# Kernel optimization log

Measured on AMD Instinct MI355X. Metric: run time of the kernel, lower is better.

Reference implementation:

```python
import jax, jax.numpy as jnp
import numpy as np


def setup_inputs() -> dict:
    key = jax.random.key(0)
    k1, k2, k3, k4 = jax.random.split(key, 4)
    B, G, C, T = 4, 40, 13, 1024
    return {
        "x": jax.random.normal(k1, (B, G, C, T), dtype=jnp.float32),
        "query_w": jax.random.normal(k2, (C, C), dtype=jnp.float32),
        "key_w": jax.random.normal(k3, (C, C), dtype=jnp.float32),
        "value_w": jax.random.normal(k4, (C, C), dtype=jnp.float32),
    }


def reference(x, query_w, key_w, value_w):
    # x: [B, 40, 13, T] real -> rfft over time -> [B, 40, 13, F] complex
    x_fft = jnp.fft.rfft(x, axis=-1)
    cdt = x_fft.dtype
    wq = query_w.astype(cdt)  # [13,13] complex (zero imag), shared across the 40 groups
    wk = key_w.astype(cdt)
    wv = value_w.astype(cdt)
    xt = jnp.swapaxes(x_fft, -1, -2)  # [B, 40, F, 13]
    q = xt @ wq                       # [B, 40, F, 13]
    k = xt @ wk
    v = xt @ wv
    scores = jnp.abs(q @ jnp.swapaxes(k, -1, -2))     # [B, 40, F, F] real
    attn = jax.nn.softmax(scores, axis=-1).astype(cdt)
    out = (attn @ v)                                   # [B, 40, F, 13]
    out = jnp.swapaxes(out, -1, -2)                    # [B, 40, 13, F]
    return jnp.fft.irfft(out, axis=-1)                 # [B, 40, 13, 2*(F-1)]
```

## Files before the change

kernel.cpp:

```cpp
#include <hip/hip_runtime.h>
#include <math.h>

#define BDIM 4
#define GDIM 40
#define CDIM 13
#define TDIM 1024
#define FDIM 513
#define BG   (BDIM*GDIM)
#define NROW (BG*FDIM)
#define NCHUNK 9
#define TK 64

typedef _Float16 half4 __attribute__((ext_vector_type(4)));
typedef _Float16 half8 __attribute__((ext_vector_type(8)));
typedef float    f32x4 __attribute__((ext_vector_type(4)));

#define MFMA16(a, b, c) __builtin_amdgcn_mfma_f32_16x16x16f16((a), (b), (c), 0, 0, 0)

__device__ __forceinline__ unsigned bitrev10(unsigned x) { return __brev(x) >> 22; }

__global__ void fft_fwd2(const float* __restrict__ x, float2* __restrict__ xf) {
    __shared__ float re[1024], im[1024];
    const int s2 = blockIdx.x;
    const float* x1 = x + (size_t)(2 * s2) * TDIM;
    const float* x2 = x1 + TDIM;
    for (int t = threadIdx.x; t < 1024; t += blockDim.x) {
        unsigned r = bitrev10(t);
        re[r] = x1[t];
        im[r] = x2[t];
    }
    __syncthreads();
    for (int s = 0; s < 10; ++s) {
        int half = 1 << s;
        for (int j = threadIdx.x; j < 512; j += blockDim.x) {
            int grp = j >> s;
            int pos = j & (half - 1);
            int i1 = (grp << (s + 1)) + pos;
            int i2 = i1 + half;
            float ang = -(float)M_PI * (float)pos / (float)half;
            float sw, cw; __sincosf(ang, &sw, &cw);
            float xr = re[i2], xi = im[i2];
            float tr = cw * xr - sw * xi;
            float ti = cw * xi + sw * xr;
            float ur = re[i1], ui = im[i1];
            re[i1] = ur + tr; im[i1] = ui + ti;
            re[i2] = ur - tr; im[i2] = ui - ti;
        }
        __syncthreads();
    }
    const int sigA = 2 * s2, sigB = sigA + 1;
    const int bgA = sigA / CDIM, cA = sigA % CDIM;
    const int bgB = sigB / CDIM, cB = sigB % CDIM;
    for (int f = threadIdx.x; f < FDIM; f += blockDim.x) {
        int fr = (1024 - f) & 1023;
        float zr = re[f], zi = im[f];
        float wr = re[fr], wi = im[fr];
        xf[((size_t)bgA * FDIM + f) * CDIM + cA] =
            make_float2(0.5f * (zr + wr), 0.5f * (zi - wi));
        xf[((size_t)bgB * FDIM + f) * CDIM + cB] =
            make_float2(0.5f * (zi + wi), 0.5f * (wr - zr));
    }
}

__global__ void qkv_kernel(const float2* __restrict__ xf,
                           const float* __restrict__ wq,
                           const float* __restrict__ wk,
                           const float* __restrict__ wv,
                           float2* __restrict__ q,
                           _Float16* __restrict__ KP,
                           _Float16* __restrict__ VT) {
    int gid = blockIdx.x * blockDim.x + threadIdx.x;
    if (gid >= NROW * CDIM) return;
    int r = gid / CDIM;
    int i = gid - r * CDIM;
    const float2* xrow = xf + (size_t)r * CDIM;
    float qr = 0, qi = 0, kr = 0, ki = 0, vr = 0, vi = 0;
#pragma unroll
    for (int c = 0; c < CDIM; ++c) {
        float2 xc = xrow[c];
        float a = wq[c * CDIM + i]; qr += xc.x * a; qi += xc.y * a;
        float b = wk[c * CDIM + i]; kr += xc.x * b; ki += xc.y * b;
        float d = wv[c * CDIM + i]; vr += xc.x * d; vi += xc.y * d;
    }
    q[gid] = make_float2(qr, qi);

    _Float16* krow = KP + (size_t)r * 64;
    _Float16 h0 = (_Float16)kr;
    _Float16 h1 = (_Float16)ki;
    krow[i]      = h0;
    krow[13 + i] = h1;
    krow[32 + i] = (_Float16)(kr - (float)h0);
    krow[45 + i] = (_Float16)(ki - (float)h1);
    if (i == 12) {
        *(unsigned int*)(krow + 26) = 0u;
        *(unsigned int*)(krow + 28) = 0u;
        *(unsigned int*)(krow + 30) = 0u;
        *(unsigned int*)(krow + 58) = 0u;
        *(unsigned int*)(krow + 60) = 0u;
        *(unsigned int*)(krow + 62) = 0u;
    }
    int bg = r / FDIM;
    int f  = r - bg * FDIM;
    VT[((size_t)(bg * 2 + 0) * 16 + i) * 520 + f] = (_Float16)vr;
    VT[((size_t)(bg * 2 + 1) * 16 + i) * 520 + f] = (_Float16)vi;
}

__global__ __launch_bounds__(256, 4) void attn_kernel(const float2* __restrict__ q,
                                                      const _Float16* __restrict__ KP,
                                                      const _Float16* __restrict__ VT,
                                                      float2* __restrict__ outspec) {
    __shared__ __align__(16) _Float16 Klds[TK * 64];
    __shared__ __align__(16) _Float16 VTlds[2 * 16 * 72];

    const int bg    = blockIdx.x / NCHUNK;
    const int chunk = blockIdx.x % NCHUNK;
    const int tid   = threadIdx.x;
    const int w     = tid >> 6;
    const int lane  = tid & 63;
    const int qlane = lane & 15;
    const int g     = lane >> 4;
    const int frow  = chunk * 64 + w * 16 + qlane;
    const bool writer = (frow < FDIM);
    const int f     = writer ? frow : (FDIM - 1);
    const size_t rowbase = (size_t)(bg * FDIM + f) * CDIM;

    half4 uh[2], ul[2], u2h[2], u2l[2];
#pragma unroll
    for (int c01 = 0; c01 < 2; ++c01) {
#pragma unroll
        for (int j = 0; j < 4; ++j) {
            int k = c01 * 16 + 4 * g + j;
            float a = 0.f, b = 0.f;
            if (k < CDIM) {
                float2 t = q[rowbase + k];          a = t.x;  b = t.y;
            } else if (k < 2 * CDIM) {
                float2 t = q[rowbase + (k - CDIM)]; a = -t.y; b = t.x;
            }
            _Float16 ah = (_Float16)a;
            uh[c01][j]  = ah;
            ul[c01][j]  = (_Float16)(a - (float)ah);
            _Float16 bh = (_Float16)b;
            u2h[c01][j] = bh;
            u2l[c01][j] = (_Float16)(b - (float)bh);
        }
    }

    f32x4 o_re = {0.f, 0.f, 0.f, 0.f};
    f32x4 o_im = {0.f, 0.f, 0.f, 0.f};
    float m = -INFINITY, l = 0.f;

    const _Float16* __restrict__ KPg = KP + (size_t)bg * FDIM * 64;
    const _Float16* __restrict__ VTg = VT + (size_t)bg * 2 * 16 * 520;

    for (int t0 = 0; t0 < FDIM; t0 += TK) {
        __syncthreads();
#pragma unroll
        for (int hh = 0; hh < 2; ++hh) {
            int gr  = tid + hh * 256;
            int krw = gr >> 3, gg = gr & 7;
            half8 val;
#pragma unroll
            for (int e = 0; e < 8; ++e) val[e] = (_Float16)0.f;
            int grow = t0 + krw;
            if (grow < FDIM)
                val = *(const half8*)(KPg + (size_t)grow * 64 + gg * 8);
            *(half8*)(Klds + krw * 64 + ((gg ^ (krw & 7)) << 3)) = val;
        }
        {
            int gk = tid & 7, cc = (tid >> 3) & 15, part = tid >> 7;
            int rb = t0 + gk * 8;
            half8 val;
#pragma unroll
            for (int e = 0; e < 8; ++e) val[e] = (_Float16)0.f;
            if (rb < FDIM) {
                val = *(const half8*)(VTg + ((size_t)(part * 16 + cc)) * 520 + rb);
                if (rb + 8 > FDIM) {
#pragma unroll
                    for (int e = 0; e < 8; ++e) if (rb + e >= FDIM) val[e] = (_Float16)0.f;
                }
            }
            *(half8*)(VTlds + (part * 16 + cc) * 72 + gk * 8) = val;
        }
        __syncthreads();

#pragma unroll
        for (int sub = 0; sub < 4; ++sub) {
            const int arow = sub * 16 + qlane;
            const int rx   = arow & 7;
            const _Float16* kr = Klds + arow * 64;
#define KFRAG(h) (*(const half4*)(kr + (((((h) >> 3)) ^ rx) << 3) + ((h) & 7)))
            half4 wh0 = KFRAG(4 * g);
            half4 wh1 = KFRAG(16 + 4 * g);
            half4 wl0 = KFRAG(32 + 4 * g);
            half4 wl1 = KFRAG(48 + 4 * g);
#undef KFRAG
            f32x4 sre = {0.f, 0.f, 0.f, 0.f};
            f32x4 sim = {0.f, 0.f, 0.f, 0.f};
            sre = MFMA16(wh0, uh[0], sre);
            sre = MFMA16(wh1, uh[1], sre);
            sre = MFMA16(wl0, uh[0], sre);
            sre = MFMA16(wl1, uh[1], sre);
            sre = MFMA16(wh0, ul[0], sre);
            sre = MFMA16(wh1, ul[1], sre);
            sre = MFMA16(wl0, ul[0], sre);
            sre = MFMA16(wl1, ul[1], sre);
            sim = MFMA16(wh0, u2h[0], sim);
            sim = MFMA16(wh1, u2h[1], sim);
            sim = MFMA16(wl0, u2h[0], sim);
            sim = MFMA16(wl1, u2h[1], sim);
            sim = MFMA16(wh0, u2l[0], sim);
            sim = MFMA16(wh1, u2l[1], sim);
            sim = MFMA16(wl0, u2l[0], sim);
            sim = MFMA16(wl1, u2l[1], sim);

            float s0 = sqrtf(fmaf(sre[0], sre[0], sim[0] * sim[0]));
            float s1 = sqrtf(fmaf(sre[1], sre[1], sim[1] * sim[1]));
            float s2 = sqrtf(fmaf(sre[2], sre[2], sim[2] * sim[2]));
            float s3 = sqrtf(fmaf(sre[3], sre[3], sim[3] * sim[3]));
            float tmax = fmaxf(fmaxf(s0, s1), fmaxf(s2, s3));
            tmax = fmaxf(tmax, __shfl_xor(tmax, 16));
            tmax = fmaxf(tmax, __shfl_xor(tmax, 32));
            float mnew  = fmaxf(m, tmax);
            float alpha = __expf(m - mnew);
            m = mnew;
            l *= alpha;
            o_re *= alpha;
            o_im *= alpha;
            float p0 = __expf(s0 - m);
            float p1 = __expf(s1 - m);
            float p2 = __expf(s2 - m);
            float p3 = __expf(s3 - m);
            l += (p0 + p1) + (p2 + p3);
            half4 pk;
            pk[0] = (_Float16)p0; pk[1] = (_Float16)p1;
            pk[2] = (_Float16)p2; pk[3] = (_Float16)p3;

            const int voff = sub * 16 + 4 * g;
            half4 vfr = *(const half4*)(VTlds + qlane * 72 + voff);
            half4 vfi = *(const half4*)(VTlds + (16 + qlane) * 72 + voff);
            o_re = MFMA16(vfr, pk, o_re);
            o_im = MFMA16(vfi, pk, o_im);
        }
    }

    l += __shfl_xor(l, 16);
    l += __shfl_xor(l, 32);
    if (writer) {
        float inv = 1.f / l;
#pragma unroll
        for (int j = 0; j < 4; ++j) {
            int c = 4 * g + j;
            if (c < CDIM)
                outspec[((size_t)(bg * CDIM + c)) * FDIM + frow] =
                    make_float2(o_re[j] * inv, o_im[j] * inv);
        }
    }
}

__global__ void fft_inv2(const float2* __restrict__ spec, float* __restrict__ out) {
    __shared__ float re[1024], im[1024];
    const int s2 = blockIdx.x;
    const float2* Y1 = spec + (size_t)(2 * s2) * FDIM;
    const float2* Y2 = Y1 + FDIM;
    for (int t = threadIdx.x; t < 1024; t += blockDim.x) {
        float a, b, c, d;
        if (t <= 512) {
            float2 y1 = Y1[t], y2 = Y2[t];
            bool edge = (t == 0) | (t == 512);
            a = y1.x; b = edge ? 0.f : y1.y;
            c = y2.x; d = edge ? 0.f : y2.y;
        } else {
            float2 y1 = Y1[1024 - t], y2 = Y2[1024 - t];
            a = y1.x; b = -y1.y;
            c = y2.x; d = -y2.y;
        }
        unsigned r = bitrev10(t);
        re[r] = a - d;
        im[r] = b + c;
    }
    __syncthreads();
    for (int s = 0; s < 10; ++s) {
        int half = 1 << s;
        for (int j = threadIdx.x; j < 512; j += blockDim.x) {
            int grp = j >> s;
            int pos = j & (half - 1);
            int i1 = (grp << (s + 1)) + pos;
            int i2 = i1 + half;
            float ang = (float)M_PI * (float)pos / (float)half;
            float sw, cw; __sincosf(ang, &sw, &cw);
            float xr = re[i2], xi = im[i2];
            float tr = cw * xr - sw * xi;
            float ti = cw * xi + sw * xr;
            float ur = re[i1], ui = im[i1];
            re[i1] = ur + tr; im[i1] = ui + ti;
            re[i2] = ur - tr; im[i2] = ui - ti;
        }
        __syncthreads();
    }
    const float scale = 1.0f / 1024.0f;
    float* o1 = out + (size_t)(2 * s2) * TDIM;
    for (int t = threadIdx.x; t < 1024; t += blockDim.x) {
        o1[t]        = re[t] * scale;
        o1[TDIM + t] = im[t] * scale;
    }
}

extern "C" void kernel_launch(void* const* d_in, const int* in_sizes, int n_in,
                              void* d_out, int out_size, void* d_ws, size_t ws_size,
                              hipStream_t stream) {
    const float* x  = (const float*)d_in[0];
    const float* wq = (const float*)d_in[1];
    const float* wk = (const float*)d_in[2];
    const float* wv = (const float*)d_in[3];
    float* out = (float*)d_out;

    const size_t n = (size_t)NROW * CDIM;
    float2* xf = (float2*)d_ws;
    float2* q  = xf + n;
    _Float16* KP = (_Float16*)(q + n);
    _Float16* VT = KP + (size_t)NROW * 64;

    fft_fwd2<<<BG * CDIM / 2, 256, 0, stream>>>(x, xf);
    qkv_kernel<<<(NROW * CDIM + 255) / 256, 256, 0, stream>>>(xf, wq, wk, wv, q, KP, VT);
    attn_kernel<<<BG * NCHUNK, 256, 0, stream>>>(q, KP, VT, xf );
    fft_inv2<<<BG * CDIM / 2, 256, 0, stream>>>(xf, out);
}
```

Before: 194.3 us.

## Split key range across wave pairs, use 16x16x32 MFMA, lazy softmax rescale

Reorganizes the attention kernel so each wave handles two query sub-tiles and the key tiles are split between two wave groups, with two K/V tiles staged per iteration. The partial softmax states are merged through LDS at the end. Score computation moves from 16x16x16 to 16x16x32 MFMA, halving the instruction count. Max rescaling is skipped when the new max stays within a threshold of the running max. The intent is to raise MFMA throughput and cut rescale work, at the cost of more registers and LDS, a final merge step, and a changed occupancy hint.

```diff
diff --git a/kernel.cpp b/kernel.cpp
--- a/kernel.cpp
+++ b/kernel.cpp
@@ -16,6 +16,7 @@
 typedef float    f32x4 __attribute__((ext_vector_type(4)));
 
 #define MFMA16(a, b, c) __builtin_amdgcn_mfma_f32_16x16x16f16((a), (b), (c), 0, 0, 0)
+#define MFMA32(a, b, c) __builtin_amdgcn_mfma_f32_16x16x32_f16((a), (b), (c), 0, 0, 0)
 
 __device__ __forceinline__ unsigned bitrev10(unsigned x) { return __brev(x) >> 22; }
 
@@ -105,12 +106,12 @@
     VT[((size_t)(bg * 2 + 1) * 16 + i) * 520 + f] = (_Float16)vi;
 }
 
-__global__ __launch_bounds__(256, 4) void attn_kernel(const float2* __restrict__ q,
+__global__ __launch_bounds__(256, 5) void attn_kernel(const float2* __restrict__ q,
                                                       const _Float16* __restrict__ KP,
                                                       const _Float16* __restrict__ VT,
                                                       float2* __restrict__ outspec) {
-    __shared__ __align__(16) _Float16 Klds[TK * 64];
-    __shared__ __align__(16) _Float16 VTlds[2 * 16 * 72];
+    __shared__ __align__(16) _Float16 Klds[2 * TK * 64];
+    __shared__ __align__(16) _Float16 VTlds[2 * 2 * 16 * 72];
 
     const int bg    = blockIdx.x / NCHUNK;
     const int chunk = blockIdx.x % NCHUNK;
@@ -119,140 +120,210 @@
     const int lane  = tid & 63;
     const int qlane = lane & 15;
     const int g     = lane >> 4;
-    const int frow  = chunk * 64 + w * 16 + qlane;
-    const bool writer = (frow < FDIM);
-    const int f     = writer ? frow : (FDIM - 1);
-    const size_t rowbase = (size_t)(bg * FDIM + f) * CDIM;
-
-    half4 uh[2], ul[2], u2h[2], u2l[2];
-#pragma unroll
-    for (int c01 = 0; c01 < 2; ++c01) {
-#pragma unroll
-        for (int j = 0; j < 4; ++j) {
-            int k = c01 * 16 + 4 * g + j;
-            float a = 0.f, b = 0.f;
-            if (k < CDIM) {
-                float2 t = q[rowbase + k];          a = t.x;  b = t.y;
-            } else if (k < 2 * CDIM) {
-                float2 t = q[rowbase + (k - CDIM)]; a = -t.y; b = t.x;
-            }
-            _Float16 ah = (_Float16)a;
-            uh[c01][j]  = ah;
-            ul[c01][j]  = (_Float16)(a - (float)ah);
-            _Float16 bh = (_Float16)b;
-            u2h[c01][j] = bh;
-            u2l[c01][j] = (_Float16)(b - (float)bh);
-        }
-    }
-
-    f32x4 o_re = {0.f, 0.f, 0.f, 0.f};
-    f32x4 o_im = {0.f, 0.f, 0.f, 0.f};
-    float m = -INFINITY, l = 0.f;
+    const int qpair = w & 1;
+    const int kh    = w >> 1;
+
+    half8 Quh[2], Qul[2], Qu2h[2], Qu2l[2];
+    int   frow_s[2];
+#pragma unroll
+    for (int s = 0; s < 2; ++s) {
+        frow_s[s] = chunk * 64 + (qpair * 2 + s) * 16 + qlane;
+        const int f = (frow_s[s] < FDIM) ? frow_s[s] : (FDIM - 1);
+        const size_t rowbase = ((size_t)bg * FDIM + f) * CDIM;
+#pragma unroll
+        for (int c = 0; c < 2; ++c) {
+#pragma unroll
+            for (int j = 0; j < 4; ++j) {
+                const int e = 4 * c + j;
+                const int k = 16 * c + 4 * g + j;
+                float a = 0.f, b = 0.f;
+                if (k < CDIM) {
+                    float2 t = q[rowbase + k];          a = t.x;  b = t.y;
+                } else if (k < 2 * CDIM) {
+                    float2 t = q[rowbase + (k - CDIM)]; a = -t.y; b = t.x;
+                }
+                _Float16 ah = (_Float16)a;
+                Quh[s][e]  = ah;
+                Qul[s][e]  = (_Float16)(a - (float)ah);
+                _Float16 bh = (_Float16)b;
+                Qu2h[s][e] = bh;
+                Qu2l[s][e] = (_Float16)(b - (float)bh);
+            }
+        }
+    }
+
+    f32x4 ore[2], oim[2];
+    float m[2], l[2];
+#pragma unroll
+    for (int s = 0; s < 2; ++s) {
+        ore[s] = (f32x4){0.f, 0.f, 0.f, 0.f};
+        oim[s] = (f32x4){0.f, 0.f, 0.f, 0.f};
+        m[s] = -INFINITY; l[s] = 0.f;
+    }
 
     const _Float16* __restrict__ KPg = KP + (size_t)bg * FDIM * 64;
     const _Float16* __restrict__ VTg = VT + (size_t)bg * 2 * 16 * 520;
-
-    for (int t0 = 0; t0 < FDIM; t0 += TK) {
+    const _Float16* KB = Klds  + kh * (TK * 64);
+    const _Float16* VB = VTlds + kh * (2 * 16 * 72);
+
+    for (int it = 0; it < 5; ++it) {
         __syncthreads();
 #pragma unroll
-        for (int hh = 0; hh < 2; ++hh) {
-            int gr  = tid + hh * 256;
-            int krw = gr >> 3, gg = gr & 7;
-            half8 val;
-#pragma unroll
-            for (int e = 0; e < 8; ++e) val[e] = (_Float16)0.f;
-            int grow = t0 + krw;
-            if (grow < FDIM)
-                val = *(const half8*)(KPg + (size_t)grow * 64 + gg * 8);
-            *(half8*)(Klds + krw * 64 + ((gg ^ (krw & 7)) << 3)) = val;
-        }
-        {
-            int gk = tid & 7, cc = (tid >> 3) & 15, part = tid >> 7;
-            int rb = t0 + gk * 8;
-            half8 val;
-#pragma unroll
-            for (int e = 0; e < 8; ++e) val[e] = (_Float16)0.f;
-            if (rb < FDIM) {
-                val = *(const half8*)(VTg + ((size_t)(part * 16 + cc)) * 520 + rb);
-                if (rb + 8 > FDIM) {
-#pragma unroll
-                    for (int e = 0; e < 8; ++e) if (rb + e >= FDIM) val[e] = (_Float16)0.f;
-                }
-            }
-            *(half8*)(VTlds + (part * 16 + cc) * 72 + gk * 8) = val;
+        for (int h = 0; h < 4; ++h) {
+            int gidx = tid + h * 256;
+            int b  = gidx >> 9;
+            int g2 = gidx & 511;
+            int t  = 2 * it + b;
+            if (t <= 8) {
+                int krw = g2 >> 3, gg = g2 & 7;
+                half8 val;
+#pragma unroll
+                for (int e = 0; e < 8; ++e) val[e] = (_Float16)0.f;
+                int grow = t * TK + krw;
+                if (grow < FDIM)
+                    val = *(const half8*)(KPg + (size_t)grow * 64 + gg * 8);
+                *(half8*)(Klds + b * (TK * 64) + krw * 64 + ((gg ^ (krw & 7)) << 3)) = val;
+            }
+        }
+#pragma unroll
+        for (int h = 0; h < 2; ++h) {
+            int gidx = tid + h * 256;
+            int b  = gidx >> 8;
+            int g2 = gidx & 255;
+            int t  = 2 * it + b;
+            if (t <= 8) {
+                int part = g2 >> 7, cc = (g2 >> 3) & 15, gk = g2 & 7;
+                int rb = t * TK + gk * 8;
+                half8 val;
+#pragma unroll
+                for (int e = 0; e < 8; ++e) val[e] = (_Float16)0.f;
+                if (rb < FDIM) {
+                    val = *(const half8*)(VTg + ((size_t)(part * 16 + cc)) * 520 + rb);
+                    if (rb + 8 > FDIM) {
+#pragma unroll
+                        for (int e = 0; e < 8; ++e) if (rb + e >= FDIM) val[e] = (_Float16)0.f;
+                    }
+                }
+                *(half8*)(VTlds + b * (2 * 16 * 72) + (part * 16 + cc) * 72 + gk * 8) = val;
+            }
         }
         __syncthreads();
 
-#pragma unroll
-        for (int sub = 0; sub < 4; ++sub) {
-            const int arow = sub * 16 + qlane;
-            const int rx   = arow & 7;
-            const _Float16* kr = Klds + arow * 64;
-#define KFRAG(h) (*(const half4*)(kr + (((((h) >> 3)) ^ rx) << 3) + ((h) & 7)))
-            half4 wh0 = KFRAG(4 * g);
-            half4 wh1 = KFRAG(16 + 4 * g);
-            half4 wl0 = KFRAG(32 + 4 * g);
-            half4 wl1 = KFRAG(48 + 4 * g);
+        const int t = 2 * it + kh;
+        if (t <= 8) {
+#pragma unroll
+            for (int sub = 0; sub < 4; ++sub) {
+                const int arow = sub * 16 + qlane;
+                const int rx   = arow & 7;
+                const _Float16* kr = KB + arow * 64;
+#define KFRAG(h) (*(const half4*)(kr + ((((h) >> 3) ^ rx) << 3) + ((h) & 7)))
+                half4 a0 = KFRAG(4 * g);
+                half4 a1 = KFRAG(16 + 4 * g);
+                half4 a2 = KFRAG(32 + 4 * g);
+                half4 a3 = KFRAG(48 + 4 * g);
 #undef KFRAG
-            f32x4 sre = {0.f, 0.f, 0.f, 0.f};
-            f32x4 sim = {0.f, 0.f, 0.f, 0.f};
-            sre = MFMA16(wh0, uh[0], sre);
-            sre = MFMA16(wh1, uh[1], sre);
-            sre = MFMA16(wl0, uh[0], sre);
-            sre = MFMA16(wl1, uh[1], sre);
-            sre = MFMA16(wh0, ul[0], sre);
-            sre = MFMA16(wh1, ul[1], sre);
-            sre = MFMA16(wl0, ul[0], sre);
-            sre = MFMA16(wl1, ul[1], sre);
-            sim = MFMA16(wh0, u2h[0], sim);
-            sim = MFMA16(wh1, u2h[1], sim);
-            sim = MFMA16(wl0, u2h[0], sim);
-            sim = MFMA16(wl1, u2h[1], sim);
-            sim = MFMA16(wh0, u2l[0], sim);
-            sim = MFMA16(wh1, u2l[1], sim);
-            sim = MFMA16(wl0, u2l[0], sim);
-            sim = MFMA16(wl1, u2l[1], sim);
-
-            float s0 = sqrtf(fmaf(sre[0], sre[0], sim[0] * sim[0]));
-            float s1 = sqrtf(fmaf(sre[1], sre[1], sim[1] * sim[1]));
-            float s2 = sqrtf(fmaf(sre[2], sre[2], sim[2] * sim[2]));
-            float s3 = sqrtf(fmaf(sre[3], sre[3], sim[3] * sim[3]));
-            float tmax = fmaxf(fmaxf(s0, s1), fmaxf(s2, s3));
-            tmax = fmaxf(tmax, __shfl_xor(tmax, 16));
-            tmax = fmaxf(tmax, __shfl_xor(tmax, 32));
-            float mnew  = fmaxf(m, tmax);
-            float alpha = __expf(m - mnew);
-            m = mnew;
-            l *= alpha;
-            o_re *= alpha;
-            o_im *= alpha;
-            float p0 = __expf(s0 - m);
-            float p1 = __expf(s1 - m);
-            float p2 = __expf(s2 - m);
-            float p3 = __expf(s3 - m);
-            l += (p0 + p1) + (p2 + p3);
-            half4 pk;
-            pk[0] = (_Float16)p0; pk[1] = (_Float16)p1;
-            pk[2] = (_Float16)p2; pk[3] = (_Float16)p3;
-
-            const int voff = sub * 16 + 4 * g;
-            half4 vfr = *(const half4*)(VTlds + qlane * 72 + voff);
-            half4 vfi = *(const half4*)(VTlds + (16 + qlane) * 72 + voff);
-            o_re = MFMA16(vfr, pk, o_re);
-            o_im = MFMA16(vfi, pk, o_im);
-        }
-    }
-
-    l += __shfl_xor(l, 16);
-    l += __shfl_xor(l, 32);
-    if (writer) {
-        float inv = 1.f / l;
-#pragma unroll
-        for (int j = 0; j < 4; ++j) {
-            int c = 4 * g + j;
-            if (c < CDIM)
-                outspec[((size_t)(bg * CDIM + c)) * FDIM + frow] =
-                    make_float2(o_re[j] * inv, o_im[j] * inv);
+                half8 whh, wll;
+#pragma unroll
+                for (int j = 0; j < 4; ++j) {
+                    whh[j] = a0[j]; whh[4 + j] = a1[j];
+                    wll[j] = a2[j]; wll[4 + j] = a3[j];
+                }
+
+                float sv[2][4], tmax[2];
+#pragma unroll
+                for (int s = 0; s < 2; ++s) {
+                    f32x4 sre = {0.f, 0.f, 0.f, 0.f};
+                    f32x4 sim = {0.f, 0.f, 0.f, 0.f};
+                    sre = MFMA32(whh, Quh[s], sre);
+                    sre = MFMA32(wll, Quh[s], sre);
+                    sre = MFMA32(whh, Qul[s], sre);
+                    sre = MFMA32(wll, Qul[s], sre);
+                    sim = MFMA32(whh, Qu2h[s], sim);
+                    sim = MFMA32(wll, Qu2h[s], sim);
+                    sim = MFMA32(whh, Qu2l[s], sim);
+                    sim = MFMA32(wll, Qu2l[s], sim);
+                    sv[s][0] = sqrtf(fmaf(sre[0], sre[0], sim[0] * sim[0]));
+                    sv[s][1] = sqrtf(fmaf(sre[1], sre[1], sim[1] * sim[1]));
+                    sv[s][2] = sqrtf(fmaf(sre[2], sre[2], sim[2] * sim[2]));
+                    sv[s][3] = sqrtf(fmaf(sre[3], sre[3], sim[3] * sim[3]));
+                    float tm = fmaxf(fmaxf(sv[s][0], sv[s][1]), fmaxf(sv[s][2], sv[s][3]));
+                    tm = fmaxf(tm, __shfl_xor(tm, 16));
+                    tm = fmaxf(tm, __shfl_xor(tm, 32));
+                    tmax[s] = tm;
+                }
+                if (!__all((tmax[0] <= m[0] + 8.f) & (tmax[1] <= m[1] + 8.f))) {
+#pragma unroll
+                    for (int s = 0; s < 2; ++s) {
+                        float mnew  = fmaxf(m[s], tmax[s]);
+                        float alpha = __expf(m[s] - mnew);
+                        l[s]  *= alpha;
+                        ore[s] *= alpha;
+                        oim[s] *= alpha;
+                        m[s] = mnew;
+                    }
+                }
+                const int voff = sub * 16 + 4 * g;
+                half4 vfr = *(const half4*)(VB + qlane * 72 + voff);
+                half4 vfi = *(const half4*)(VB + (16 + qlane) * 72 + voff);
+#pragma unroll
+                for (int s = 0; s < 2; ++s) {
+                    float p0 = __expf(sv[s][0] - m[s]);
+                    float p1 = __expf(sv[s][1] - m[s]);
+                    float p2 = __expf(sv[s][2] - m[s]);
+                    float p3 = __expf(sv[s][3] - m[s]);
+                    l[s] += (p0 + p1) + (p2 + p3);
+                    half4 pk;
+                    pk[0] = (_Float16)p0; pk[1] = (_Float16)p1;
+                    pk[2] = (_Float16)p2; pk[3] = (_Float16)p3;
+                    ore[s] = MFMA16(vfr, pk, ore[s]);
+                    oim[s] = MFMA16(vfi, pk, oim[s]);
+                }
+            }
+        }
+    }
+
+    __syncthreads();
+    float* MB = (float*)Klds;
+    if (kh == 1) {
+        float* dst = MB + (qpair * 64 + lane) * 20;
+#pragma unroll
+        for (int s = 0; s < 2; ++s) {
+            dst[10 * s + 0] = m[s];
+            dst[10 * s + 1] = l[s];
+#pragma unroll
+            for (int j = 0; j < 4; ++j) {
+                dst[10 * s + 2 + j] = ore[s][j];
+                dst[10 * s + 6 + j] = oim[s][j];
+            }
+        }
+    }
+    __syncthreads();
+    if (kh == 0) {
+        const float* src = MB + (qpair * 64 + lane) * 20;
+#pragma unroll
+        for (int s = 0; s < 2; ++s) {
+            float mp = src[10 * s + 0], lp = src[10 * s + 1];
+            float M  = fmaxf(m[s], mp);
+            float sa = __expf(m[s] - M), sb = __expf(mp - M);
+            l[s] = l[s] * sa + lp * sb;
+#pragma unroll
+            for (int j = 0; j < 4; ++j) {
+                ore[s][j] = ore[s][j] * sa + src[10 * s + 2 + j] * sb;
+                oim[s][j] = oim[s][j] * sa + src[10 * s + 6 + j] * sb;
+            }
+            float lt = l[s];
+            lt += __shfl_xor(lt, 16);
+            lt += __shfl_xor(lt, 32);
+            if (frow_s[s] < FDIM) {
+                float inv = 1.f / lt;
+#pragma unroll
+                for (int j = 0; j < 4; ++j) {
+                    int c = 4 * g + j;
+                    if (c < CDIM)
+                        outspec[((size_t)(bg * CDIM + c)) * FDIM + frow_s[s]] =
+                            make_float2(ore[s][j] * inv, oim[s][j] * inv);
+                }
+            }
         }
     }
 }
```

After: 218.3 us. 12.4% more time.

## Stage QKV projection through shared memory with coalesced K/V-transpose writes

Applied to the files above, without the earlier changes.

The QKV kernel is restructured so each block handles a 64-frequency chunk of one (b,g) slice. It loads the inputs and all three weight matrices into shared memory, builds the K split-fp16 rows and the V transpose in LDS, then writes them out with 16-byte vector stores instead of scattered strided half stores. The aim is to remove the uncoalesced VT transpose writes and the repeated global weight reads. Separately, both FFT kernels now launch with 512 threads instead of 256. The QKV grid shrinks to 1440 blocks, which may reduce parallelism.

```diff
diff --git a/kernel.cpp b/kernel.cpp
--- a/kernel.cpp
+++ b/kernel.cpp
@@ -10,6 +10,7 @@
 #define NROW (BG*FDIM)
 #define NCHUNK 9
 #define TK 64
+#define QW 64
 
 typedef _Float16 half4 __attribute__((ext_vector_type(4)));
 typedef _Float16 half8 __attribute__((ext_vector_type(8)));
@@ -62,47 +63,82 @@
     }
 }
 
-__global__ void qkv_kernel(const float2* __restrict__ xf,
+__global__ __launch_bounds__(256) void qkv_kernel(const float2* __restrict__ xf,
                            const float* __restrict__ wq,
                            const float* __restrict__ wk,
                            const float* __restrict__ wv,
                            float2* __restrict__ q,
                            _Float16* __restrict__ KP,
                            _Float16* __restrict__ VT) {
-    int gid = blockIdx.x * blockDim.x + threadIdx.x;
-    if (gid >= NROW * CDIM) return;
-    int r = gid / CDIM;
-    int i = gid - r * CDIM;
-    const float2* xrow = xf + (size_t)r * CDIM;
-    float qr = 0, qi = 0, kr = 0, ki = 0, vr = 0, vi = 0;
-#pragma unroll
-    for (int c = 0; c < CDIM; ++c) {
-        float2 xc = xrow[c];
-        float a = wq[c * CDIM + i]; qr += xc.x * a; qi += xc.y * a;
-        float b = wk[c * CDIM + i]; kr += xc.x * b; ki += xc.y * b;
-        float d = wv[c * CDIM + i]; vr += xc.x * d; vi += xc.y * d;
-    }
-    q[gid] = make_float2(qr, qi);
-
-    _Float16* krow = KP + (size_t)r * 64;
-    _Float16 h0 = (_Float16)kr;
-    _Float16 h1 = (_Float16)ki;
-    krow[i]      = h0;
-    krow[13 + i] = h1;
-    krow[32 + i] = (_Float16)(kr - (float)h0);
-    krow[45 + i] = (_Float16)(ki - (float)h1);
-    if (i == 12) {
-        *(unsigned int*)(krow + 26) = 0u;
-        *(unsigned int*)(krow + 28) = 0u;
-        *(unsigned int*)(krow + 30) = 0u;
-        *(unsigned int*)(krow + 58) = 0u;
-        *(unsigned int*)(krow + 60) = 0u;
-        *(unsigned int*)(krow + 62) = 0u;
-    }
-    int bg = r / FDIM;
-    int f  = r - bg * FDIM;
-    VT[((size_t)(bg * 2 + 0) * 16 + i) * 520 + f] = (_Float16)vr;
-    VT[((size_t)(bg * 2 + 1) * 16 + i) * 520 + f] = (_Float16)vi;
+    __shared__ float2   Xs[QW * CDIM];
+    __shared__ float    Ws[3 * CDIM * CDIM];
+    __shared__ _Float16 KPs[QW * 72];
+    __shared__ _Float16 VTs[32 * 72];
+
+    const int bg    = blockIdx.x / NCHUNK;
+    const int ch    = blockIdx.x % NCHUNK;
+    const int f0    = ch * QW;
+    const int nrows = min(QW, FDIM - f0);
+    const int tid   = threadIdx.x;
+    const int nitems = nrows * CDIM;
+
+    for (int idx = tid; idx < nitems; idx += 256)
+        Xs[idx] = xf[((size_t)bg * FDIM + f0) * CDIM + idx];
+    for (int idx = tid; idx < 3 * 169; idx += 256)
+        Ws[idx] = (idx < 169) ? wq[idx] : ((idx < 338) ? wk[idx - 169] : wv[idx - 338]);
+    for (int z = tid; z < 6 * QW; z += 256) {
+        int rr = z >> 6, jj = z & 63;
+        int pc = (rr < 3) ? (13 + rr) : (29 + (rr - 3));
+        VTs[pc * 72 + jj] = (_Float16)0.f;
+    }
+    __syncthreads();
+
+    for (int item = tid; item < nitems; item += 256) {
+        int row = item / CDIM;
+        int i   = item - row * CDIM;
+        const float2* xrow = &Xs[row * CDIM];
+        float qr = 0, qi = 0, kr = 0, ki = 0, vr = 0, vi = 0;
+#pragma unroll
+        for (int c = 0; c < CDIM; ++c) {
+            float2 xc = xrow[c];
+            float a = Ws[c * CDIM + i];       qr += xc.x * a; qi += xc.y * a;
+            float b = Ws[169 + c * CDIM + i]; kr += xc.x * b; ki += xc.y * b;
+            float d = Ws[338 + c * CDIM + i]; vr += xc.x * d; vi += xc.y * d;
+        }
+        q[((size_t)bg * FDIM + f0) * CDIM + item] = make_float2(qr, qi);
+        _Float16* kp = KPs + row * 72;
+        _Float16 h0 = (_Float16)kr, h1 = (_Float16)ki;
+        kp[i]      = h0;
+        kp[13 + i] = h1;
+        kp[32 + i] = (_Float16)(kr - (float)h0);
+        kp[45 + i] = (_Float16)(ki - (float)h1);
+        if (i == 12) {
+            *(unsigned*)(kp + 26) = 0u; *(unsigned*)(kp + 28) = 0u; *(unsigned*)(kp + 30) = 0u;
+            *(unsigned*)(kp + 58) = 0u; *(unsigned*)(kp + 60) = 0u; *(unsigned*)(kp + 62) = 0u;
+        }
+        VTs[i * 72 + row]        = (_Float16)vr;
+        VTs[(16 + i) * 72 + row] = (_Float16)vi;
+    }
+    __syncthreads();
+
+    _Float16* KPg = KP + ((size_t)bg * FDIM + f0) * 64;
+    _Float16* VTg = VT + (size_t)bg * 2 * 16 * 520 + f0;
+    if (nrows == QW) {
+        for (int idx = tid; idx < QW * 8; idx += 256) {
+            int row = idx >> 3, gg = idx & 7;
+            *(half8*)(KPg + row * 64 + gg * 8) = *(const half8*)(KPs + row * 72 + gg * 8);
+        }
+        for (int idx = tid; idx < 32 * 8; idx += 256) {
+            int pc = idx >> 3, j8 = idx & 7;
+            *(half8*)(VTg + pc * 520 + j8 * 8) = *(const half8*)(VTs + pc * 72 + j8 * 8);
+        }
+    } else {
+        for (int idx = tid; idx < nrows * 8; idx += 256) {
+            int row = idx >> 3, gg = idx & 7;
+            *(half8*)(KPg + row * 64 + gg * 8) = *(const half8*)(KPs + row * 72 + gg * 8);
+        }
+        if (tid < 32) VTg[tid * 520] = VTs[tid * 72];
+    }
 }
 
 __global__ __launch_bounds__(256, 4) void attn_kernel(const float2* __restrict__ q,
@@ -122,7 +158,7 @@
     const int frow  = chunk * 64 + w * 16 + qlane;
     const bool writer = (frow < FDIM);
     const int f     = writer ? frow : (FDIM - 1);
-    const size_t rowbase = (size_t)(bg * FDIM + f) * CDIM;
+    const size_t rowbase = ((size_t)bg * FDIM + f) * CDIM;
 
     half4 uh[2], ul[2], u2h[2], u2l[2];
 #pragma unroll
@@ -320,8 +356,8 @@
     _Float16* KP = (_Float16*)(q + n);
     _Float16* VT = KP + (size_t)NROW * 64;
 
-    fft_fwd2<<<BG * CDIM / 2, 256, 0, stream>>>(x, xf);
-    qkv_kernel<<<(NROW * CDIM + 255) / 256, 256, 0, stream>>>(xf, wq, wk, wv, q, KP, VT);
+    fft_fwd2<<<BG * CDIM / 2, 512, 0, stream>>>(x, xf);
+    qkv_kernel<<<BG * NCHUNK, 256, 0, stream>>>(xf, wq, wk, wv, q, KP, VT);
     attn_kernel<<<BG * NCHUNK, 256, 0, stream>>>(q, KP, VT, xf );
-    fft_inv2<<<BG * CDIM / 2, 256, 0, stream>>>(xf, out);
-}
+    fft_inv2<<<BG * CDIM / 2, 512, 0, stream>>>(xf, out);
+}
```

Result: faster. 178.9 us (-7.9%).
